# Kernel tuning notes

Measured on AMD Instinct MI355X. Metric: run time of the kernel, lower is better.

The kernel has to match this reference:

```python
import jax, jax.numpy as jnp
import numpy as np

B, S, D = 8, 1024, 1024      # batch, seq_len, inp_dim
H, HD = 8, 64                # head_num, head_dim
HID = H * HD                 # hidden_dim = 512
P = 2 * D                    # p_factor * inp_dim = 2048
K = 4                        # causal conv kernel size
EPS = 1e-6
CAP = 15.0                   # soft cap for i/f gates


def _layernorm(x, g, b):
    mu = jnp.mean(x, -1, keepdims=True)
    var = jnp.var(x, -1, keepdims=True)
    return (x - mu) * jax.lax.rsqrt(var + EPS) * g + b


def _soft_cap(v):
    return CAP * jnp.tanh(v / CAP)


def _causal_conv_feat(x, w, b):
    # Conv1d(1,1,K) applied over the FEATURE axis of each timestep (as in the
    # torch code: x_t.unsqueeze(1) -> (bs,1,P)), causal left pad of K-1.
    L = x.shape[-1]
    xp = jnp.pad(x, ((0, 0), (0, 0), (K - 1, 0)))
    out = b
    for m in range(K):
        out = out + w[m] * xp[..., m:m + L]
    return out


def _forward(x, ln_g, ln_b, mh_g, mh_b, W_up_l, b_up_l, W_up_r, b_up_r,
             W_down, b_down, conv_w, conv_b, W_skip, b_skip, W_i, b_i,
             W_f, b_f, W_o, b_o, W_q, b_q, W_k, b_k, W_v, b_v):
    Bs, Sl, _ = x.shape
    xn = _layernorm(x, ln_g, ln_b)
    x_t = xn @ W_up_l.T + b_up_l                      # (B,S,P)
    r_t = xn @ W_up_r.T + b_up_r                      # (B,S,HID)
    x_c = jax.nn.silu(_causal_conv_feat(x_t, conv_w, conv_b))
    x_skip = x_c @ W_skip.T + b_skip                  # (B,S,HID)
    q = (x_c @ W_q.T + b_q).reshape(Bs, Sl, H, HD)
    k = (x_c @ W_k.T + b_k).reshape(Bs, Sl, H, HD) / float(np.sqrt(HD))
    v = (x_t @ W_v.T + b_v).reshape(Bs, Sl, H, HD)
    i_pre = _soft_cap(x_c @ W_i.T + b_i)              # (B,S,H)
    f_pre = _soft_cap(x_c @ W_f.T + b_f)              # (B,S,H)
    o = jax.nn.sigmoid(x_t @ W_o.T + b_o)             # (B,S,HID)

    def step(carry, inp):
        c, n, m = carry
        qt, kt, vt, it, ft = inp
        m_t = jnp.maximum(ft + m, it)
        ie = jnp.exp(it - m_t)
        fe = jnp.exp(ft - m_t + m)
        c = fe[:, :, None, None] * c + ie[:, :, None, None] * jnp.einsum('bhd,bhe->bhde', vt, kt)
        n = fe[:, :, None] * n + ie[:, :, None] * kt
        num = jnp.einsum('bhde,bhe->bhd', c, qt)
        den = jnp.maximum(jnp.sum(n * qt, -1, keepdims=True), 1.0)
        return (c, n, m_t), num / den

    c0 = jnp.zeros((Bs, H, HD, HD), x.dtype)
    n0 = jnp.ones((Bs, H, HD), x.dtype)
    m0 = jnp.zeros((Bs, H), x.dtype)
    seq = tuple(jnp.moveaxis(a, 1, 0) for a in (q, k, v, i_pre, f_pre))
    _, hs = jax.lax.scan(step, (c0, n0, m0), seq)     # hs: (S,B,H,HD)
    h = o * jnp.moveaxis(hs, 0, 1).reshape(Bs, Sl, HID)
    hn = _layernorm(h.reshape(Bs, Sl, H, HD), mh_g, mh_b).reshape(Bs, Sl, HID)
    out = (hn + x_skip) * jax.nn.silu(r_t)
    return out @ W_down.T + b_down + x


def setup_inputs() -> dict:
    key = jax.random.key(0)
    ks = jax.random.split(key, 16)

    def w(kk, shape):
        return jax.random.normal(kk, shape, jnp.float32) / np.sqrt(shape[-1]).astype(np.float32)

    return {
        'x': jax.random.normal(ks[0], (B, S, D), jnp.float32),
        'ln_g': jnp.ones((D,), jnp.float32), 'ln_b': jnp.zeros((D,), jnp.float32),
        'mh_g': jnp.ones((H, HD), jnp.float32), 'mh_b': jnp.zeros((H, HD), jnp.float32),
        'W_up_l': w(ks[1], (P, D)), 'b_up_l': jnp.zeros((P,), jnp.float32),
        'W_up_r': w(ks[2], (HID, D)), 'b_up_r': jnp.zeros((HID,), jnp.float32),
        'W_down': w(ks[3], (D, HID)), 'b_down': jnp.zeros((D,), jnp.float32),
        'conv_w': jax.random.normal(ks[4], (K,), jnp.float32) * 0.3,
        'conv_b': jnp.zeros((), jnp.float32),
        'W_skip': w(ks[5], (HID, P)), 'b_skip': jnp.zeros((HID,), jnp.float32),
        'W_i': w(ks[6], (H, P)), 'b_i': jnp.zeros((H,), jnp.float32),
        'W_f': w(ks[7], (H, P)), 'b_f': jnp.zeros((H,), jnp.float32),
        'W_o': w(ks[8], (HID, P)), 'b_o': jnp.zeros((HID,), jnp.float32),
        'W_q': w(ks[9], (HID, P)), 'b_q': jnp.zeros((HID,), jnp.float32),
        'W_k': w(ks[10], (HID, P)), 'b_k': jnp.zeros((HID,), jnp.float32),
        'W_v': w(ks[11], (HID, P)), 'b_v': jnp.zeros((HID,), jnp.float32),
    }


def reference(x, ln_g, ln_b, mh_g, mh_b, W_up_l, b_up_l, W_up_r, b_up_r,
              W_down, b_down, conv_w, conv_b, W_skip, b_skip, W_i, b_i,
              W_f, b_f, W_o, b_o, W_q, b_q, W_k, b_k, W_v, b_v):
    return _forward(x, ln_g, ln_b, mh_g, mh_b, W_up_l, b_up_l, W_up_r, b_up_r,
                    W_down, b_down, conv_w, conv_b, W_skip, b_skip, W_i, b_i,
                    W_f, b_f, W_o, b_o, W_q, b_q, W_k, b_k, W_v, b_v)
```

## Files before the change

kernel.cpp:

```cpp
#include <hip/hip_runtime.h>
#include <hip/hip_bf16.h>
#include <math.h>

#define Bq 8
#define Sq 1024
#define Dq 1024
#define Hq 8
#define HDq 64
#define HIDq 512
#define Pq 2048
#define EPSq 1e-6f
#define CAPq 15.0f
#define NCq 16
#define CLq 64
#define LDST 40
#define ARENA (128 * LDST)
#define GEMM_SMEM_BYTES (2 * 4 * ARENA * 2)

typedef __attribute__((ext_vector_type(8))) short short8;
typedef __attribute__((ext_vector_type(4))) float f32x4v;
typedef __hip_bfloat16 bf16;

__device__ inline void split2(float v, bf16& h, bf16& l) {
  h = __float2bfloat16(v);
  l = __float2bfloat16(v - __bfloat162float(h));
}

__device__ inline float bfs2f(short s) {
  bf16 t = *(const bf16*)&s;
  return __bfloat162float(t);
}

__global__ __launch_bounds__(256) void cvtw_all(
    const float* __restrict__ s0, const float* __restrict__ s1,
    const float* __restrict__ s2, const float* __restrict__ s3,
    const float* __restrict__ s4, const float* __restrict__ s5,
    const float* __restrict__ s6, const float* __restrict__ s7,
    bf16* __restrict__ hi, bf16* __restrict__ lo)
{
  int u = blockIdx.x * 256 + threadIdx.x;
  const float* src; int segBase;
  if      (u <  524288) { src = s0; segBase = 0;       }
  else if (u <  655360) { src = s1; segBase = 524288;  }
  else if (u <  917504) { src = s2; segBase = 655360;  }
  else if (u < 1179648) { src = s3; segBase = 917504;  }
  else if (u < 1441792) { src = s4; segBase = 1179648; }
  else if (u < 1703936) { src = s5; segBase = 1441792; }
  else if (u < 1966080) { src = s6; segBase = 1703936; }
  else                  { src = s7; segBase = 1966080; }
  float4 v = ((const float4*)src)[u - segBase];
  size_t o = (size_t)u * 4;
  bf16 h, l;
  split2(v.x, h, l); hi[o+0] = h; lo[o+0] = l;
  split2(v.y, h, l); hi[o+1] = h; lo[o+1] = l;
  split2(v.z, h, l); hi[o+2] = h; lo[o+2] = l;
  split2(v.w, h, l); hi[o+3] = h; lo[o+3] = l;
}

__global__ __launch_bounds__(256) void ln_kernel(const float* __restrict__ x,
    const float* __restrict__ g, const float* __restrict__ b,
    bf16* __restrict__ yh, bf16* __restrict__ yl)
{
  int row = blockIdx.x;
  int tid = threadIdx.x;
  const float* xr = x + (size_t)row * Dq;
  float v[4]; float s = 0.f, s2 = 0.f;
  #pragma unroll
  for (int i = 0; i < 4; i++) { v[i] = xr[tid + 256*i]; s += v[i]; s2 += v[i]*v[i]; }
  #pragma unroll
  for (int mm = 32; mm > 0; mm >>= 1) { s += __shfl_xor(s, mm, 64); s2 += __shfl_xor(s2, mm, 64); }
  __shared__ float rs[4], rs2[4];
  int lane = tid & 63, wave = tid >> 6;
  if (lane == 0) { rs[wave] = s; rs2[wave] = s2; }
  __syncthreads();
  s  = rs[0] + rs[1] + rs[2] + rs[3];
  s2 = rs2[0] + rs2[1] + rs2[2] + rs2[3];
  float mu  = s * (1.f / Dq);
  float var = s2 * (1.f / Dq) - mu * mu;
  float r = rsqrtf(var + EPSq);
  #pragma unroll
  for (int i = 0; i < 4; i++) {
    int c = tid + 256*i;
    float y = (v[i] - mu) * r * g[c] + b[c];
    bf16 h, l; split2(y, h, l);
    yh[(size_t)row * Dq + c] = h;
    yl[(size_t)row * Dq + c] = l;
  }
}

__global__ __launch_bounds__(256) void gemm_x3(
    const bf16* __restrict__ Ahi, const bf16* __restrict__ Alo,
    const bf16* __restrict__ Whi, const bf16* __restrict__ Wlo,
    int Kd, int start1, int start2, const float* __restrict__ resid,
    const float* bias0, float* f0, bf16* h0, bf16* l0, int w0, float sc0, int a0,
    const float* bias1, float* f1, bf16* h1, bf16* l1, int w1, float sc1, int a1,
    const float* bias2, float* f2, bf16* h2, bf16* l2, int w2, float sc2, int a2)
{
  extern __shared__ short smem[];
  int tid = threadIdx.x;
  int lane = tid & 63, wave = tid >> 6;
  int wr = wave >> 1, wc = wave & 1;

  int gx = gridDim.x;
  int flat = blockIdx.y * gx + blockIdx.x;
  int nb = gx * gridDim.y;
  int chunk = nb >> 3;
  int nid = (flat & 7) * chunk + (flat >> 3);
  int col = nid % gx, row = nid / gx;
  int rowBase = row * 128;
  int colBase = col * 128;

  int sk  = (tid & 3) * 8;
  int sr0 = tid >> 2;
  int sr1 = 64 + sr0;

  const short* Ahg = (const short*)Ahi + (size_t)rowBase * Kd;
  const short* Alg = (const short*)Alo + (size_t)rowBase * Kd;
  const short* Bhg = (const short*)Whi + (size_t)colBase * Kd;
  const short* Blg = (const short*)Wlo + (size_t)colBase * Kd;

  f32x4v acc[4][4];
  #pragma unroll
  for (int i = 0; i < 4; i++)
    #pragma unroll
    for (int j = 0; j < 4; j++) acc[i][j] = (f32x4v){0.f, 0.f, 0.f, 0.f};

  int fk = (lane >> 4) * 8;
  int fr = lane & 15;
  int nk = Kd >> 5;

  short8 ah0, ah1, al0, al1, bh0, bh1, bl0, bl1;

#define LOAD_TILE(k0) do {                                                    \
    size_t o0 = (size_t)sr0 * Kd + (k0) + sk;                                 \
    size_t o1 = (size_t)sr1 * Kd + (k0) + sk;                                 \
    ah0 = *(const short8*)(Ahg + o0); ah1 = *(const short8*)(Ahg + o1);       \
    al0 = *(const short8*)(Alg + o0); al1 = *(const short8*)(Alg + o1);       \
    bh0 = *(const short8*)(Bhg + o0); bh1 = *(const short8*)(Bhg + o1);       \
    bl0 = *(const short8*)(Blg + o0); bl1 = *(const short8*)(Blg + o1);       \
  } while (0)

#define STORE_TILE(S) do {                                                    \
    *(short8*)&(S)[0*ARENA + sr0*LDST + sk] = ah0;                            \
    *(short8*)&(S)[0*ARENA + sr1*LDST + sk] = ah1;                            \
    *(short8*)&(S)[1*ARENA + sr0*LDST + sk] = al0;                            \
    *(short8*)&(S)[1*ARENA + sr1*LDST + sk] = al1;                            \
    *(short8*)&(S)[2*ARENA + sr0*LDST + sk] = bh0;                            \
    *(short8*)&(S)[2*ARENA + sr1*LDST + sk] = bh1;                            \
    *(short8*)&(S)[3*ARENA + sr0*LDST + sk] = bl0;                            \
    *(short8*)&(S)[3*ARENA + sr1*LDST + sk] = bl1;                            \
  } while (0)

  LOAD_TILE(0);
  STORE_TILE(smem);
  if (nk > 1) LOAD_TILE(32);
  asm volatile("s_waitcnt lgkmcnt(0)" ::: "memory");
  __builtin_amdgcn_s_barrier();

  for (int t = 0; t < nk; ++t) {
    const short* C = smem + (t & 1) * (4 * ARENA);
    short* Nx      = smem + ((t + 1) & 1) * (4 * ARENA);

    short8 afh[4], afl[4], bfh[4], bfl[4];
    #pragma unroll
    for (int mi = 0; mi < 4; mi++) {
      afh[mi] = *(const short8*)&C[0*ARENA + (wr * 64 + mi * 16 + fr) * LDST + fk];
      afl[mi] = *(const short8*)&C[1*ARENA + (wr * 64 + mi * 16 + fr) * LDST + fk];
    }
    #pragma unroll
    for (int ni = 0; ni < 4; ni++) {
      bfh[ni] = *(const short8*)&C[2*ARENA + (wc * 64 + ni * 16 + fr) * LDST + fk];
      bfl[ni] = *(const short8*)&C[3*ARENA + (wc * 64 + ni * 16 + fr) * LDST + fk];
    }
    __builtin_amdgcn_sched_barrier(0);
    if (t + 1 < nk) STORE_TILE(Nx);
    __builtin_amdgcn_sched_barrier(0);
    if (t + 2 < nk) LOAD_TILE((size_t)(t + 2) << 5);
    __builtin_amdgcn_sched_barrier(0);
    __builtin_amdgcn_s_setprio(1);
    #pragma unroll
    for (int mi = 0; mi < 4; mi++)
      #pragma unroll
      for (int ni = 0; ni < 4; ni++)
        acc[mi][ni] = __builtin_amdgcn_mfma_f32_16x16x32_bf16(afh[mi], bfh[ni], acc[mi][ni], 0, 0, 0);
    #pragma unroll
    for (int mi = 0; mi < 4; mi++)
      #pragma unroll
      for (int ni = 0; ni < 4; ni++)
        acc[mi][ni] = __builtin_amdgcn_mfma_f32_16x16x32_bf16(afh[mi], bfl[ni], acc[mi][ni], 0, 0, 0);
    #pragma unroll
    for (int mi = 0; mi < 4; mi++)
      #pragma unroll
      for (int ni = 0; ni < 4; ni++)
        acc[mi][ni] = __builtin_amdgcn_mfma_f32_16x16x32_bf16(afl[mi], bfh[ni], acc[mi][ni], 0, 0, 0);
    __builtin_amdgcn_s_setprio(0);
    asm volatile("s_waitcnt lgkmcnt(0)" ::: "memory");
    __builtin_amdgcn_sched_barrier(0);
    __builtin_amdgcn_s_barrier();
  }
#undef LOAD_TILE
#undef STORE_TILE

  const float* bias; float* fOut; bf16* hOut; bf16* lOut; int segStart, segW; float sscale; int sact;
  if (colBase >= start2)      { bias=bias2; fOut=f2; hOut=h2; lOut=l2; segStart=start2; segW=w2; sscale=sc2; sact=a2; }
  else if (colBase >= start1) { bias=bias1; fOut=f1; hOut=h1; lOut=l1; segStart=start1; segW=w1; sscale=sc1; sact=a1; }
  else                        { bias=bias0; fOut=f0; hOut=h0; lOut=l0; segStart=0;      segW=w0; sscale=sc0; sact=a0; }

  int cr = (lane >> 4) * 4;
  int cc = lane & 15;
  #pragma unroll
  for (int mi = 0; mi < 4; mi++) {
    #pragma unroll
    for (int ni = 0; ni < 4; ni++) {
      int colO  = colBase + wc * 64 + ni * 16 + cc;
      int colL = colO - segStart;
      float bv = bias[colL];
      #pragma unroll
      for (int j = 0; j < 4; j++) {
        int rowO = rowBase + wr * 64 + mi * 16 + cr + j;
        float val = (acc[mi][ni][j] + bv) * sscale;
        if (sact) val = 1.f / (1.f + expf(-val));
        if (resid && segStart == 0) val += resid[(size_t)rowO * segW + colL];
        size_t oidx = (size_t)rowO * segW + colL;
        if (fOut) fOut[oidx] = val;
        if (hOut) {
          bf16 h, l; split2(val, h, l);
          hOut[oidx] = h; lOut[oidx] = l;
        }
      }
    }
  }
}

__global__ __launch_bounds__(256) void conv_kernel(const bf16* __restrict__ xth,
    const bf16* __restrict__ xtl, const float* __restrict__ cw,
    const float* __restrict__ cb, bf16* __restrict__ xch, bf16* __restrict__ xcl,
    int total8)
{
  int u = blockIdx.x * 256 + threadIdx.x;
  if (u >= total8) return;
  size_t idx = (size_t)u * 8;
  int p0 = (int)(idx & (Pq - 1));
  const short* hp = (const short*)xth + idx;
  const short* lp = (const short*)xtl + idx;
  short8 ch = *(const short8*)hp;
  short8 cl = *(const short8*)lp;
  float xv[11];
  #pragma unroll
  for (int j = 0; j < 8; j++) xv[3 + j] = bfs2f(ch[j]) + bfs2f(cl[j]);
  if (p0 > 0) {
    short8 ph = *(const short8*)(hp - 8);
    short8 pl = *(const short8*)(lp - 8);
    xv[0] = bfs2f(ph[5]) + bfs2f(pl[5]);
    xv[1] = bfs2f(ph[6]) + bfs2f(pl[6]);
    xv[2] = bfs2f(ph[7]) + bfs2f(pl[7]);
  } else {
    xv[0] = xv[1] = xv[2] = 0.f;
  }
  float w0 = cw[0], w1 = cw[1], w2 = cw[2], w3 = cw[3], bb = cb[0];
  short8 oh, ol;
  #pragma unroll
  for (int j = 0; j < 8; j++) {
    float acc = bb + w3 * xv[j + 3] + w2 * xv[j + 2] + w1 * xv[j + 1] + w0 * xv[j];
    float y = acc / (1.f + expf(-acc));
    bf16 h, l; split2(y, h, l);
    oh[j] = *(const short*)&h;
    ol[j] = *(const short*)&l;
  }
  *(short8*)((short*)xch + idx) = oh;
  *(short8*)((short*)xcl + idx) = ol;
}

__global__ __launch_bounds__(256) void ifk_kernel(const bf16* __restrict__ xch,
    const bf16* __restrict__ xcl,
    const float* __restrict__ Wi, const float* __restrict__ bi,
    const float* __restrict__ Wf, const float* __restrict__ bf_,
    float* __restrict__ ip, float* __restrict__ fp)
{
  int row = blockIdx.x;
  int lane = threadIdx.x & 63, wave = threadIdx.x >> 6;
  size_t rb = (size_t)row * Pq;
  const short* xh = (const short*)xch + rb;
  const short* xl = (const short*)xcl + rb;
  for (int oi = wave; oi < 16; oi += 4) {
    int hh = oi & 7;
    const float* Wrow = (oi < 8) ? (Wi + (size_t)hh * Pq) : (Wf + (size_t)hh * Pq);
    float s = 0.f;
    for (int j0 = lane * 8; j0 < Pq; j0 += 512) {
      short8 hv = *(const short8*)(xh + j0);
      short8 lv = *(const short8*)(xl + j0);
      float4 wa = *(const float4*)(Wrow + j0);
      float4 wb = *(const float4*)(Wrow + j0 + 4);
      s += (bfs2f(hv[0]) + bfs2f(lv[0])) * wa.x;
      s += (bfs2f(hv[1]) + bfs2f(lv[1])) * wa.y;
      s += (bfs2f(hv[2]) + bfs2f(lv[2])) * wa.z;
      s += (bfs2f(hv[3]) + bfs2f(lv[3])) * wa.w;
      s += (bfs2f(hv[4]) + bfs2f(lv[4])) * wb.x;
      s += (bfs2f(hv[5]) + bfs2f(lv[5])) * wb.y;
      s += (bfs2f(hv[6]) + bfs2f(lv[6])) * wb.z;
      s += (bfs2f(hv[7]) + bfs2f(lv[7])) * wb.w;
    }
    #pragma unroll
    for (int mm = 32; mm > 0; mm >>= 1) s += __shfl_xor(s, mm, 64);
    if (lane == 0) {
      float val = s + ((oi < 8) ? bi[hh] : bf_[hh]);
      val = CAPq * tanhf(val / CAPq);
      if (oi < 8) ip[(size_t)row * Hq + hh] = val;
      else        fp[(size_t)row * Hq + hh] = val;
    }
  }
}

__global__ __launch_bounds__(256) void chunkA_kernel(const float* __restrict__ k,
    const float* __restrict__ v, const float* __restrict__ ip,
    const float* __restrict__ fp, float* __restrict__ bg,
    float* __restrict__ FcMc, float* __restrict__ kvg, float* __restrict__ ksumg)
{
  int blk = blockIdx.x;
  int bh = blk >> 4, c = blk & 15;
  int b = bh >> 3, hh = bh & 7;
  int tid = threadIdx.x, lane = tid & 63, wave = tid >> 6;

  __shared__ float sK[64][64], sV[64][64], sW[64];

  size_t base = (size_t)b * Sq * 512 + (size_t)hh * 64 + (size_t)c * CLq * 512;
  int tr = tid >> 4, c4 = (tid & 15) * 4;
  #pragma unroll
  for (int p = 0; p < 4; p++) {
    int t = p * 16 + tr;
    *(float4*)&sK[t][c4] = *(const float4*)(k + base + (size_t)t * 512 + c4);
    *(float4*)&sV[t][c4] = *(const float4*)(v + base + (size_t)t * 512 + c4);
  }
  if (tid < 64) {
    size_t ifb = ((size_t)b * Sq + c * CLq + tid) * Hq + hh;
    float fv = fp[ifb], iv = ip[ifb];
    float cf = fv;
    #pragma unroll
    for (int off = 1; off < 64; off <<= 1) {
      float t2 = __shfl_up(cf, off, 64);
      if (lane >= off) cf += t2;
    }
    float bs = iv - cf;
    float mx = bs;
    #pragma unroll
    for (int off = 1; off < 64; off <<= 1) {
      float t2 = __shfl_up(mx, off, 64);
      if (lane >= off) mx = fmaxf(mx, t2);
    }
    float Mc = __shfl(mx, 63, 64);
    bg[(size_t)blk * 64 + tid] = bs;
    sW[tid] = expf(bs - Mc);
    if (tid == 63) { FcMc[blk*2] = cf; FcMc[blk*2+1] = Mc; }
  }
  __syncthreads();
  float acc[16];
  #pragma unroll
  for (int j = 0; j < 16; j++) acc[j] = 0.f;
  for (int s = 0; s < 64; s++) {
    float wv = sW[s] * sV[s][lane];
    #pragma unroll
    for (int j = 0; j < 16; j++) acc[j] += wv * sK[s][wave*16+j];
  }
  float* kvp = kvg + (size_t)blk * 4096 + lane * 64 + wave * 16;
  #pragma unroll
  for (int j = 0; j < 16; j++) kvp[j] = acc[j];
  if (tid < 64) {
    float a = 0.f;
    for (int s = 0; s < 64; s++) a += sW[s] * sK[s][tid];
    ksumg[(size_t)blk * 64 + tid] = a;
  }
}

__global__ __launch_bounds__(1024) void chunkB_kernel(const float* __restrict__ kvg,
    const float* __restrict__ ksumg, const float* __restrict__ FcMc,
    float* __restrict__ boundC, float* __restrict__ boundN, float* __restrict__ boundM)
{
  int bh = blockIdx.x;
  int tid = threadIdx.x;
  int r  = tid >> 4;
  int cq = (tid & 15) * 4;
  float4 C4 = {0.f, 0.f, 0.f, 0.f};
  float ne = 1.0f, m = 0.f;
  for (int c = 0; c < NCq; c++) {
    size_t blk = (size_t)bh * NCq + c;
    *(float4*)(boundC + blk * 4096 + r * 64 + cq) = C4;
    if ((tid & 15) == 0) boundN[blk * 64 + r] = ne;
    if (tid == 0)        boundM[blk] = m;
    float Fc = FcMc[blk * 2], Mc = FcMc[blk * 2 + 1];
    float mm = fmaxf(m, Mc);
    float a1 = expf(m - mm), a2 = expf(Mc - mm);
    float4 kv = *(const float4*)(kvg + blk * 4096 + r * 64 + cq);
    C4.x = a1 * C4.x + a2 * kv.x;
    C4.y = a1 * C4.y + a2 * kv.y;
    C4.z = a1 * C4.z + a2 * kv.z;
    C4.w = a1 * C4.w + a2 * kv.w;
    ne = a1 * ne + a2 * ksumg[blk * 64 + r];
    m = Fc + mm;
  }
}

__global__ __launch_bounds__(256) void chunkC_kernel(const float* q,
    const float* __restrict__ k, const float* __restrict__ v,
    const float* __restrict__ bg, const float* __restrict__ boundC,
    const float* __restrict__ boundN, const float* __restrict__ boundM,
    float* hs)
{
  int blk = blockIdx.x;
  int bh = blk >> 4, c = blk & 15;
  int b = bh >> 3, hh = bh & 7;
  int tid = threadIdx.x, lane = tid & 63, wave = tid >> 6;

  __shared__ float sQ[64][65], sKV[64][65], sS[64][65];
  __shared__ float sB[64], sMr[64], sNin[64];

  size_t base = (size_t)b * Sq * 512 + (size_t)hh * 64 + (size_t)c * CLq * 512;
  int tr = tid >> 4, c4 = (tid & 15) * 4;
  #pragma unroll
  for (int p = 0; p < 4; p++) {
    int t = p * 16 + tr;
    float4 qv = *(const float4*)(q + base + (size_t)t * 512 + c4);
    float4 kv = *(const float4*)(k + base + (size_t)t * 512 + c4);
    sQ[t][c4+0] = qv.x; sQ[t][c4+1] = qv.y; sQ[t][c4+2] = qv.z; sQ[t][c4+3] = qv.w;
    sKV[t][c4+0] = kv.x; sKV[t][c4+1] = kv.y; sKV[t][c4+2] = kv.z; sKV[t][c4+3] = kv.w;
  }
  float m_in = boundM[blk];
  if (tid < 64) {
    float bs = bg[(size_t)blk * 64 + tid];
    float mx = bs;
    #pragma unroll
    for (int off = 1; off < 64; off <<= 1) {
      float t2 = __shfl_up(mx, off, 64);
      if (lane >= off) mx = fmaxf(mx, t2);
    }
    sB[tid]   = bs;
    sMr[tid]  = fmaxf(m_in, mx);
    sNin[tid] = boundN[(size_t)blk * 64 + tid];
  }
  __syncthreads();

  {
    int t = lane;
    float acc[16];
    #pragma unroll
    for (int j = 0; j < 16; j++) acc[j] = 0.f;
    for (int d = 0; d < 64; d++) {
      float qv = sQ[t][d];
      #pragma unroll
      for (int j = 0; j < 16; j++) acc[j] += qv * sKV[wave*16+j][d];
    }
    float Mr = sMr[t];
    #pragma unroll
    for (int j = 0; j < 16; j++) {
      int s = wave * 16 + j;
      float w = (s <= t) ? expf(sB[s] - Mr) : 0.f;
      sS[t][s] = w * acc[j];
    }
  }
  __syncthreads();
  #pragma unroll
  for (int p = 0; p < 4; p++) {
    int t = p * 16 + tr;
    float4 vv = *(const float4*)(v + base + (size_t)t * 512 + c4);
    sKV[t][c4+0] = vv.x; sKV[t][c4+1] = vv.y; sKV[t][c4+2] = vv.z; sKV[t][c4+3] = vv.w;
  }
  __syncthreads();

  {
    int t = lane;
    float Mr = sMr[t];
    float bfac = expf(m_in - Mr);
    float den = 0.f;
    for (int d = 0; d < 64; d++) den += sNin[d] * sQ[t][d];
    den *= bfac;
    float num[16];
    #pragma unroll
    for (int j = 0; j < 16; j++) num[j] = 0.f;
    const float* Crow = boundC + (size_t)blk * 4096;
    for (int e = 0; e < 64; e++) {
      float qv = sQ[t][e];
      #pragma unroll
      for (int j = 0; j < 16; j++)
        num[j] += Crow[(size_t)(wave*16+j) * 64 + e] * qv;
    }
    #pragma unroll
    for (int j = 0; j < 16; j++) num[j] *= bfac;
    for (int s = 0; s < 64; s++) {
      float ws = sS[t][s];
      den += ws;
      #pragma unroll
      for (int j = 0; j < 16; j++) num[j] += ws * sKV[s][wave*16+j];
    }
    den = fmaxf(den, 1.0f);
    float o[16];
    #pragma unroll
    for (int j = 0; j < 16; j++) o[j] = num[j] / den;
    float* hp = hs + base + (size_t)t * 512 + wave * 16;
    #pragma unroll
    for (int j4 = 0; j4 < 4; j4++)
      ((float4*)hp)[j4] = ((float4*)o)[j4];
  }
}

__global__ __launch_bounds__(256) void epi_kernel(const float* __restrict__ hsv,
    const float* __restrict__ ov, const float* __restrict__ xs,
    const float* __restrict__ rt, const float* __restrict__ mg,
    const float* __restrict__ mb, bf16* __restrict__ pdh, bf16* __restrict__ pdl)
{
  int tid = threadIdx.x;
  int lane = tid & 63, wave = tid >> 6;
  size_t row = (size_t)blockIdx.x * 4 + wave;
  int hh = (int)(row & 7);
  size_t idx = row * 64 + lane;
  float hv = ov[idx] * hsv[idx];
  float s = hv, s2 = hv * hv;
  #pragma unroll
  for (int mm = 32; mm > 0; mm >>= 1) { s += __shfl_xor(s, mm, 64); s2 += __shfl_xor(s2, mm, 64); }
  float mu  = s * (1.f / 64.f);
  float var = s2 * (1.f / 64.f) - mu * mu;
  float r = rsqrtf(var + EPSq);
  float hn = (hv - mu) * r * mg[hh * 64 + lane] + mb[hh * 64 + lane];
  float rv = rt[idx];
  float y = (hn + xs[idx]) * (rv / (1.f + expf(-rv)));
  bf16 h, l; split2(y, h, l);
  pdh[idx] = h; pdl[idx] = l;
}

extern "C" void kernel_launch(void* const* d_in, const int* in_sizes, int n_in,
                              void* d_out, int out_size, void* d_ws, size_t ws_size,
                              hipStream_t stream)
{
  const float* x      = (const float*)d_in[0];
  const float* ln_g   = (const float*)d_in[1];
  const float* ln_b   = (const float*)d_in[2];
  const float* mh_g   = (const float*)d_in[3];
  const float* mh_b   = (const float*)d_in[4];
  const float* W_up_l = (const float*)d_in[5];
  const float* b_up_l = (const float*)d_in[6];
  const float* W_up_r = (const float*)d_in[7];
  const float* b_up_r = (const float*)d_in[8];
  const float* W_down = (const float*)d_in[9];
  const float* b_down = (const float*)d_in[10];
  const float* conv_w = (const float*)d_in[11];
  const float* conv_b = (const float*)d_in[12];
  const float* W_skip = (const float*)d_in[13];
  const float* b_skip = (const float*)d_in[14];
  const float* W_i    = (const float*)d_in[15];
  const float* b_i    = (const float*)d_in[16];
  const float* W_f    = (const float*)d_in[17];
  const float* b_f    = (const float*)d_in[18];
  const float* W_o    = (const float*)d_in[19];
  const float* b_o    = (const float*)d_in[20];
  const float* W_q    = (const float*)d_in[21];
  const float* b_q    = (const float*)d_in[22];
  const float* W_k    = (const float*)d_in[23];
  const float* b_k    = (const float*)d_in[24];
  const float* W_v    = (const float*)d_in[25];
  const float* b_v    = (const float*)d_in[26];
  float* out = (float*)d_out;

  const size_t MB = 1u << 20;
  if (ws_size < 193 * MB) return;

  static bool attrSet = false;
  if (!attrSet) {
    (void)hipFuncSetAttribute(reinterpret_cast<const void*>(gemm_x3),
                              hipFuncAttributeMaxDynamicSharedMemorySize,
                              GEMM_SMEM_BYTES);
    attrSet = true;
  }

  char* base = (char*)d_ws;
  bf16* whi = (bf16*)base;
  bf16* wlo = (bf16*)(base + 16*MB);
  bf16* xnh = (bf16*)(base + 32*MB);
  bf16* xnl = (bf16*)(base + 48*MB);
  bf16* xth = (bf16*)(base + 64*MB);
  bf16* xtl = (bf16*)(base + 96*MB);
  bf16* xch = (bf16*)(base + 128*MB);
  bf16* xcl = (bf16*)(base + 160*MB);
  float* vb  = (float*)(base + 32*MB);
  float* ob  = (float*)(base + 48*MB);
  float* xs  = (float*)(base + 64*MB);
  float* qb  = (float*)(base + 80*MB);
  float* kb  = (float*)(base + 96*MB);
  bf16*  pdh = (bf16*)(base + 112*MB);
  bf16*  pdl = (bf16*)(base + 120*MB);
  float* kvg    = (float*)(base + 128*MB);
  float* boundC = (float*)(base + 144*MB);
  float* bg     = (float*)(base + 160*MB);
  float* ksumg  = (float*)(base + 160*MB + 256*1024);
  float* boundN = (float*)(base + 160*MB + 512*1024);
  float* FcMc   = (float*)(base + 160*MB + 768*1024);
  float* boundM = (float*)(base + 160*MB + 776*1024);
  float* ip  = (float*)(base + 192*MB);
  float* fpb = (float*)(base + 192*MB + 256*1024);
  float* rt  = out;
  float* hsb = qb;

  const int Mrows = Bq * Sq;
  const int BIG = 1 << 30;

  cvtw_all<<<dim3(8192), dim3(256), 0, stream>>>(
      W_up_l, W_up_r, W_v, W_o, W_skip, W_q, W_k, W_down, whi, wlo);

  ln_kernel<<<dim3(Mrows), dim3(256), 0, stream>>>(x, ln_g, ln_b, xnh, xnl);

  gemm_x3<<<dim3(20, 64), dim3(256), GEMM_SMEM_BYTES, stream>>>(
      xnh, xnl, whi, wlo, 1024, 2048, BIG, nullptr,
      b_up_l, nullptr, xth, xtl, 2048, 1.f, 0,
      b_up_r, rt, nullptr, nullptr, 512, 1.f, 0,
      nullptr, nullptr, nullptr, nullptr, 1, 1.f, 0);

  gemm_x3<<<dim3(8, 64), dim3(256), GEMM_SMEM_BYTES, stream>>>(
      xth, xtl, whi + 2621440, wlo + 2621440, 2048, 512, BIG, nullptr,
      b_v, vb, nullptr, nullptr, 512, 1.f, 0,
      b_o, ob, nullptr, nullptr, 512, 1.f, 1,
      nullptr, nullptr, nullptr, nullptr, 1, 1.f, 0);

  int convTotal8 = Mrows * Pq / 8;
  conv_kernel<<<dim3(convTotal8 / 256), dim3(256), 0, stream>>>(
      xth, xtl, conv_w, conv_b, xch, xcl, convTotal8);

  gemm_x3<<<dim3(12, 64), dim3(256), GEMM_SMEM_BYTES, stream>>>(
      xch, xcl, whi + 4718592, wlo + 4718592, 2048, 512, 1024, nullptr,
      b_skip, xs, nullptr, nullptr, 512, 1.f, 0,
      b_q, qb, nullptr, nullptr, 512, 1.f, 0,
      b_k, kb, nullptr, nullptr, 512, 0.125f, 0);

  ifk_kernel<<<dim3(Mrows), dim3(256), 0, stream>>>(
      xch, xcl, W_i, b_i, W_f, b_f, ip, fpb);

  chunkA_kernel<<<dim3(Bq * Hq * NCq), dim3(256), 0, stream>>>(
      kb, vb, ip, fpb, bg, FcMc, kvg, ksumg);
  chunkB_kernel<<<dim3(Bq * Hq), dim3(1024), 0, stream>>>(
      kvg, ksumg, FcMc, boundC, boundN, boundM);
  chunkC_kernel<<<dim3(Bq * Hq * NCq), dim3(256), 0, stream>>>(
      qb, kb, vb, bg, boundC, boundN, boundM, hsb);

  epi_kernel<<<dim3(Mrows * Hq / 4), dim3(256), 0, stream>>>(
      hsb, ob, xs, rt, mh_g, mh_b, pdh, pdl);

  gemm_x3<<<dim3(8, 64), dim3(256), GEMM_SMEM_BYTES, stream>>>(
      pdh, pdl, whi + 7864320, wlo + 7864320, 512, BIG, BIG, x,
      b_down, out, nullptr, nullptr, 1024, 1.f, 0,
      nullptr, nullptr, nullptr, nullptr, 1, 1.f, 0,
      nullptr, nullptr, nullptr, nullptr, 1, 1.f, 0);
}
```

Before: 866.2 us.

## Stage GEMM tiles with direct global-to-LDS loads and XOR-swizzled layout

Replaces the register-staged global load plus LDS store pipeline in the split-bf16 GEMM with global_load_lds direct copies, each wave filling one of the four operand arenas. The padded LDS row layout is replaced by a dense 32-element row with an XOR swizzle to avoid bank conflicts on fragment reads. This cuts register pressure and VALU/LDS store instructions, but drops the two-deep register prefetch and the setprio scheduling hints, so load latency may be less hidden. It also removes the dynamic shared-memory attribute call; the new 64KB requirement may or may not need it.

```diff
diff --git a/kernel.cpp b/kernel.cpp
--- a/kernel.cpp
+++ b/kernel.cpp
@@ -13,9 +13,9 @@
 #define CAPq 15.0f
 #define NCq 16
 #define CLq 64
-#define LDST 40
-#define ARENA (128 * LDST)
-#define GEMM_SMEM_BYTES (2 * 4 * ARENA * 2)
+#define ARENA_SH 4096
+#define BUF_SH   (4 * ARENA_SH)
+#define GEMM_SMEM_BYTES (2 * BUF_SH * 2)
 
 typedef __attribute__((ext_vector_type(8))) short short8;
 typedef __attribute__((ext_vector_type(4))) float f32x4v;
@@ -88,6 +88,23 @@
   }
 }
 
+__device__ __forceinline__ void stage_arena(short* ldsArena, const short* g,
+                                            int Kd, int k0, int lane)
+{
+  int rsub = lane >> 2;
+  int cs = (lane & 3) ^ ((lane >> 3) & 3);
+  const short* gp = g + (size_t)rsub * Kd + k0 + cs * 8;
+  short* lp = ldsArena;
+  #pragma unroll
+  for (int j = 0; j < 8; j++) {
+    __builtin_amdgcn_global_load_lds(
+        (const __attribute__((address_space(1))) void*)gp,
+        (__attribute__((address_space(3))) void*)lp, 16, 0, 0);
+    gp += (size_t)16 * Kd;
+    lp += 512;
+  }
+}
+
 __global__ __launch_bounds__(256) void gemm_x3(
     const bf16* __restrict__ Ahi, const bf16* __restrict__ Alo,
     const bf16* __restrict__ Whi, const bf16* __restrict__ Wlo,
@@ -110,74 +127,49 @@
   int rowBase = row * 128;
   int colBase = col * 128;
 
-  int sk  = (tid & 3) * 8;
-  int sr0 = tid >> 2;
-  int sr1 = 64 + sr0;
-
   const short* Ahg = (const short*)Ahi + (size_t)rowBase * Kd;
   const short* Alg = (const short*)Alo + (size_t)rowBase * Kd;
   const short* Bhg = (const short*)Whi + (size_t)colBase * Kd;
   const short* Blg = (const short*)Wlo + (size_t)colBase * Kd;
 
+  const short* src = (wave == 0) ? Ahg : (wave == 1) ? Alg
+                   : (wave == 2) ? Bhg : Blg;
+  short* arena0 = smem + wave * ARENA_SH;
+  short* arena1 = smem + BUF_SH + wave * ARENA_SH;
+
   f32x4v acc[4][4];
   #pragma unroll
   for (int i = 0; i < 4; i++)
     #pragma unroll
     for (int j = 0; j < 4; j++) acc[i][j] = (f32x4v){0.f, 0.f, 0.f, 0.f};
 
-  int fk = (lane >> 4) * 8;
   int fr = lane & 15;
+  int cch = lane >> 4;
+  int slotOff = ((cch ^ ((fr >> 1) & 3)) << 3);
   int nk = Kd >> 5;
 
-  short8 ah0, ah1, al0, al1, bh0, bh1, bl0, bl1;
-
-#define LOAD_TILE(k0) do {                                                    \
-    size_t o0 = (size_t)sr0 * Kd + (k0) + sk;                                 \
-    size_t o1 = (size_t)sr1 * Kd + (k0) + sk;                                 \
-    ah0 = *(const short8*)(Ahg + o0); ah1 = *(const short8*)(Ahg + o1);       \
-    al0 = *(const short8*)(Alg + o0); al1 = *(const short8*)(Alg + o1);       \
-    bh0 = *(const short8*)(Bhg + o0); bh1 = *(const short8*)(Bhg + o1);       \
-    bl0 = *(const short8*)(Blg + o0); bl1 = *(const short8*)(Blg + o1);       \
-  } while (0)
-
-#define STORE_TILE(S) do {                                                    \
-    *(short8*)&(S)[0*ARENA + sr0*LDST + sk] = ah0;                            \
-    *(short8*)&(S)[0*ARENA + sr1*LDST + sk] = ah1;                            \
-    *(short8*)&(S)[1*ARENA + sr0*LDST + sk] = al0;                            \
-    *(short8*)&(S)[1*ARENA + sr1*LDST + sk] = al1;                            \
-    *(short8*)&(S)[2*ARENA + sr0*LDST + sk] = bh0;                            \
-    *(short8*)&(S)[2*ARENA + sr1*LDST + sk] = bh1;                            \
-    *(short8*)&(S)[3*ARENA + sr0*LDST + sk] = bl0;                            \
-    *(short8*)&(S)[3*ARENA + sr1*LDST + sk] = bl1;                            \
-  } while (0)
-
-  LOAD_TILE(0);
-  STORE_TILE(smem);
-  if (nk > 1) LOAD_TILE(32);
-  asm volatile("s_waitcnt lgkmcnt(0)" ::: "memory");
+  stage_arena(arena0, src, Kd, 0, lane);
+  asm volatile("s_waitcnt vmcnt(0)" ::: "memory");
   __builtin_amdgcn_s_barrier();
 
   for (int t = 0; t < nk; ++t) {
-    const short* C = smem + (t & 1) * (4 * ARENA);
-    short* Nx      = smem + ((t + 1) & 1) * (4 * ARENA);
+    const short* Cb = smem + (t & 1) * BUF_SH;
+    short* nxt = (t & 1) ? arena0 : arena1;
+    if (t + 1 < nk) stage_arena(nxt, src, Kd, (t + 1) * 32, lane);
 
     short8 afh[4], afl[4], bfh[4], bfl[4];
     #pragma unroll
     for (int mi = 0; mi < 4; mi++) {
-      afh[mi] = *(const short8*)&C[0*ARENA + (wr * 64 + mi * 16 + fr) * LDST + fk];
-      afl[mi] = *(const short8*)&C[1*ARENA + (wr * 64 + mi * 16 + fr) * LDST + fk];
+      int Ra = (wr * 64 + mi * 16 + fr) * 32;
+      afh[mi] = *(const short8*)&Cb[0 * ARENA_SH + Ra + slotOff];
+      afl[mi] = *(const short8*)&Cb[1 * ARENA_SH + Ra + slotOff];
     }
     #pragma unroll
     for (int ni = 0; ni < 4; ni++) {
-      bfh[ni] = *(const short8*)&C[2*ARENA + (wc * 64 + ni * 16 + fr) * LDST + fk];
-      bfl[ni] = *(const short8*)&C[3*ARENA + (wc * 64 + ni * 16 + fr) * LDST + fk];
-    }
-    __builtin_amdgcn_sched_barrier(0);
-    if (t + 1 < nk) STORE_TILE(Nx);
-    __builtin_amdgcn_sched_barrier(0);
-    if (t + 2 < nk) LOAD_TILE((size_t)(t + 2) << 5);
-    __builtin_amdgcn_sched_barrier(0);
-    __builtin_amdgcn_s_setprio(1);
+      int Rb = (wc * 64 + ni * 16 + fr) * 32;
+      bfh[ni] = *(const short8*)&Cb[2 * ARENA_SH + Rb + slotOff];
+      bfl[ni] = *(const short8*)&Cb[3 * ARENA_SH + Rb + slotOff];
+    }
     #pragma unroll
     for (int mi = 0; mi < 4; mi++)
       #pragma unroll
@@ -193,13 +185,10 @@
       #pragma unroll
       for (int ni = 0; ni < 4; ni++)
         acc[mi][ni] = __builtin_amdgcn_mfma_f32_16x16x32_bf16(afl[mi], bfh[ni], acc[mi][ni], 0, 0, 0);
-    __builtin_amdgcn_s_setprio(0);
-    asm volatile("s_waitcnt lgkmcnt(0)" ::: "memory");
-    __builtin_amdgcn_sched_barrier(0);
+
+    asm volatile("s_waitcnt vmcnt(0)" ::: "memory");
     __builtin_amdgcn_s_barrier();
   }
-#undef LOAD_TILE
-#undef STORE_TILE
 
   const float* bias; float* fOut; bf16* hOut; bf16* lOut; int segStart, segW; float sscale; int sact;
   if (colBase >= start2)      { bias=bias2; fOut=f2; hOut=h2; lOut=l2; segStart=start2; segW=w2; sscale=sc2; sact=a2; }
@@ -561,14 +550,6 @@
   const size_t MB = 1u << 20;
   if (ws_size < 193 * MB) return;
 
-  static bool attrSet = false;
-  if (!attrSet) {
-    (void)hipFuncSetAttribute(reinterpret_cast<const void*>(gemm_x3),
-                              hipFuncAttributeMaxDynamicSharedMemorySize,
-                              GEMM_SMEM_BYTES);
-    attrSet = true;
-  }
-
   char* base = (char*)d_ws;
   bf16* whi = (bf16*)base;
   bf16* wlo = (bf16*)(base + 16*MB);
```

Result: faster. 843.6 us (-2.6%).
